# Kernel optimization log

Hardware: AMD Instinct MI355X
Metric: run time of the kernel (lower is better)

The kernel has to match this reference:

```python
import jax, jax.numpy as jnp
import numpy as np

N_NODES = 16384
D_FEAT = 128
HIDDEN = 64
THRESH = 0.85


def setup_inputs() -> dict:
    key = jax.random.key(0)
    kx, kw = jax.random.split(key, 2)
    x = jax.random.normal(kx, (N_NODES, D_FEAT), dtype=jnp.float32)
    # nn.Linear(node_features, hidden_size): weight [H, D], bias [H]
    W = jax.random.normal(kw, (HIDDEN, D_FEAT), dtype=jnp.float32) * 0.05
    b = jnp.zeros((HIDDEN,), dtype=jnp.float32)
    return {"x": x, "W": W, "b": b}


def reference(x, W, b):
    n = x.shape[0]
    # fidelity = (x_i . x_j)^2 for all pairs  -> [n, n]
    fid = jnp.square(x @ x.T)
    # edges exist iff fid >= threshold (weight 1.0); the 0.5-weight elif branch
    # in the original is unreachable. No self-loops (j starts at i+1).
    adj = (fid >= THRESH).astype(x.dtype)
    idx = jnp.arange(n)
    adj = adj.at[idx, idx].set(0.0)
    # weighted neighbor sum per node: [n, d]
    sums = adj @ x
    # original assigns agg[node] = (weights @ neighbor_feats).mean(), a SCALAR
    # broadcast across the feature row; isolated nodes stay zero (their sum
    # row is already zero, so mean is zero -> identical result).
    agg = jnp.broadcast_to(jnp.mean(sums, axis=-1, keepdims=True), x.shape)
    return agg @ W.T + b
```

## Files before the change

kernel.cpp:

```cpp
#include <hip/hip_runtime.h>

#define N_NODES 16384
#define D_FEAT  128
#define HIDDEN  64
#define THRESH  0.85f
#define BAND    0.004f
#define LQCAP   512
#define NBLK    512

typedef __attribute__((ext_vector_type(8))) short bf16x8;
typedef __attribute__((ext_vector_type(4))) float f32x4;

__device__ __forceinline__ unsigned short f32_to_bf16_rne(float f) {
    unsigned u = __float_as_uint(f);
    unsigned r = (u + 0x7FFFu + ((u >> 16) & 1u)) >> 16;
    return (unsigned short)r;
}

__device__ __forceinline__ void gl_lds16(const unsigned short* src, unsigned short* dst) {
    __builtin_amdgcn_global_load_lds(
        (const __attribute__((address_space(1))) unsigned int*)src,
        (__attribute__((address_space(3))) unsigned int*)dst, 16, 0, 0);
}

__global__ __launch_bounds__(256) void convert_kernel(const float* __restrict__ x,
                                                      unsigned short* __restrict__ xhi,
                                                      unsigned short* __restrict__ xlo) {
    int t = blockIdx.x * 256 + threadIdx.x;
    float4 v = ((const float4*)x)[t];
    float f[4] = {v.x, v.y, v.z, v.w};
    ushort4 ho, lo;
    unsigned short* hp = &ho.x;
    unsigned short* lp = &lo.x;
    #pragma unroll
    for (int k = 0; k < 4; ++k) {
        unsigned short h = f32_to_bf16_rne(f[k]);
        float hf = __uint_as_float(((unsigned)h) << 16);
        hp[k] = h;
        lp[k] = f32_to_bf16_rne(f[k] - hf);
    }
    ((ushort4*)xhi)[t] = ho;
    ((ushort4*)xlo)[t] = lo;
}

__global__ __launch_bounds__(256) void rowsum_kernel(const float* __restrict__ in,
                                                     float* __restrict__ out,
                                                     int nrows) {
    int wave = (blockIdx.x * blockDim.x + threadIdx.x) >> 6;
    int lane = threadIdx.x & 63;
    if (wave >= nrows) return;
    const float2 v = *reinterpret_cast<const float2*>(&in[wave * D_FEAT + lane * 2]);
    float sum = v.x + v.y;
    #pragma unroll
    for (int off = 32; off > 0; off >>= 1) sum += __shfl_down(sum, off, 64);
    if (lane == 0) out[wave] = sum;
}

__global__ __launch_bounds__(256, 2) void pair_mfma(const unsigned short* __restrict__ xhi,
                                                    const unsigned short* __restrict__ xlo,
                                                    const float* __restrict__ s,
                                                    float* __restrict__ acc,
                                                    unsigned* __restrict__ gqueue,
                                                    int* __restrict__ gqcnt) {
    __shared__ unsigned short Bs[2][2][64][128];
    __shared__ unsigned lq[LQCAP];
    __shared__ int lqcnt, lqbase;

    const int tid  = threadIdx.x;
    const int lane = tid & 63;
    const int w    = tid >> 6;
    const int l15  = lane & 15, l4 = lane >> 4, l7 = lane & 7;

    const int bid = blockIdx.x;
    const int swz = (bid & 7) * 64 + (bid >> 3);
    const int it  = swz & 63;
    const int jc  = swz >> 6;
    const int i0  = it * 256 + w * 64;
    const int jb0 = jc * 2048;

    bf16x8 ahi[4][4], alo[4][4];
    {
        const int abase = (i0 + l15) * D_FEAT + l4 * 8;
        #pragma unroll
        for (int rf = 0; rf < 4; ++rf)
            #pragma unroll
            for (int kc = 0; kc < 4; ++kc) {
                const int off = abase + rf * 16 * D_FEAT + kc * 32;
                ahi[rf][kc] = *(const bf16x8*)(xhi + off);
                alo[rf][kc] = *(const bf16x8*)(xlo + off);
            }
    }

    const int base_off = (tid >> 4) * 128 + (((tid & 15) ^ ((tid >> 4) & 7)) * 8);
    unsigned short* const dst0 = &Bs[0][0][0][0] + w * 512;

    const int rbyte = l15 * 256;
    int swzb[4];
    #pragma unroll
    for (int kc = 0; kc < 4; ++kc) swzb[kc] = (((kc * 4 + l4) ^ l7) * 16);

    {
        const int jelem = jb0 * D_FEAT;
        const unsigned short* hsrc = xhi + jelem + base_off;
        const unsigned short* lsrc = xlo + jelem + base_off;
        #pragma unroll
        for (int q = 0; q < 4; ++q) gl_lds16(hsrc + q * 2048, dst0 + q * 2048);
        #pragma unroll
        for (int q = 0; q < 4; ++q) gl_lds16(lsrc + q * 2048, dst0 + 8192 + q * 2048);
    }
    if (tid == 0) lqcnt = 0;
    __syncthreads();

    float accf[4][4] = {{0.f}};
    const char* const BsBytes = (const char*)&Bs[0][0][0][0];

    for (int jt = 0; jt < 32; ++jt) {
        const int buf = jt & 1;
        const int jb = jb0 + jt * 64;

        float sv[4];
        #pragma unroll
        for (int cg = 0; cg < 4; ++cg) sv[cg] = s[jb + cg * 16 + l15];

        if (jt < 31) {
            const int jelem = (jb + 64) * D_FEAT;
            const unsigned short* hsrc = xhi + jelem + base_off;
            const unsigned short* lsrc = xlo + jelem + base_off;
            unsigned short* db = dst0 + (buf ^ 1) * 16384;
            #pragma unroll
            for (int q = 0; q < 4; ++q) gl_lds16(hsrc + q * 2048, db + q * 2048);
            #pragma unroll
            for (int q = 0; q < 4; ++q) gl_lds16(lsrc + q * 2048, db + 8192 + q * 2048);
        }

        const bool diag = (jb == i0);
        const char* bp = BsBytes + buf * 32768;

        #pragma unroll
        for (int cg = 0; cg < 4; ++cg) {
            f32x4 C[4];
            #pragma unroll
            for (int rf = 0; rf < 4; ++rf) C[rf] = (f32x4){0.f, 0.f, 0.f, 0.f};

            #pragma unroll
            for (int kc = 0; kc < 4; ++kc) {
                const bf16x8 bh = *(const bf16x8*)(bp + cg * 4096 + rbyte + swzb[kc]);
                const bf16x8 bl = *(const bf16x8*)(bp + 16384 + cg * 4096 + rbyte + swzb[kc]);
                #pragma unroll
                for (int rf = 0; rf < 4; ++rf) {
                    C[rf] = __builtin_amdgcn_mfma_f32_16x16x32_bf16(ahi[rf][kc], bh, C[rf], 0, 0, 0);
                    C[rf] = __builtin_amdgcn_mfma_f32_16x16x32_bf16(alo[rf][kc], bh, C[rf], 0, 0, 0);
                    C[rf] = __builtin_amdgcn_mfma_f32_16x16x32_bf16(ahi[rf][kc], bl, C[rf], 0, 0, 0);
                }
            }

            const int jcol = jb + cg * 16 + l15;
            const float svc = sv[cg];
            #pragma unroll
            for (int rf = 0; rf < 4; ++rf) {
                const int gib = i0 + rf * 16 + l4 * 4;
                #pragma unroll
                for (int r = 0; r < 4; ++r) {
                    const float d = C[rf][r];
                    const float tt = fmaf(d, d, -THRESH);
                    if (fabsf(tt) < BAND) {
                        int p = atomicAdd(&lqcnt, 1);
                        if (p < LQCAP)
                            lq[p] = (((unsigned)(gib + r)) << 14) | (unsigned)jcol;
                    }
                    bool edge = (tt >= BAND);
                    if (diag) edge = edge && ((gib + r) != jcol);
                    accf[rf][r] += edge ? svc : 0.f;
                }
            }
        }
        __syncthreads();
    }

    if (tid == 0) {
        int c = lqcnt; if (c > LQCAP) c = LQCAP;
        lqbase = atomicAdd(gqcnt, c);
        lqcnt = c;
    }
    __syncthreads();
    for (int p = tid; p < lqcnt; p += 256) gqueue[lqbase + p] = lq[p];

    #pragma unroll
    for (int rf = 0; rf < 4; ++rf)
        #pragma unroll
        for (int r = 0; r < 4; ++r) {
            float v = accf[rf][r];
            v += __shfl_xor(v, 1);
            v += __shfl_xor(v, 2);
            v += __shfl_xor(v, 4);
            v += __shfl_xor(v, 8);
            if (l15 == 0) atomicAdd(&acc[i0 + rf * 16 + l4 * 4 + r], v);
        }
}

__global__ __launch_bounds__(256) void fixup_kernel(const unsigned* __restrict__ q,
                                                    const int* __restrict__ qcnt,
                                                    const float* __restrict__ x,
                                                    const float* __restrict__ s,
                                                    float* __restrict__ acc) {
    const int n = *qcnt;
    const int gw = (blockIdx.x * 256 + threadIdx.x) >> 6;
    const int lane = threadIdx.x & 63;
    const int nw = (gridDim.x * 256) >> 6;
    for (int p = gw; p < n; p += nw) {
        const unsigned e = q[p];
        const int i = (int)(e >> 14), j = (int)(e & 16383u);
        const float2 av = ((const float2*)(x + (size_t)i * D_FEAT))[lane];
        const float2 bv = ((const float2*)(x + (size_t)j * D_FEAT))[lane];
        float d = fmaf(av.y, bv.y, av.x * bv.x);
        #pragma unroll
        for (int off = 32; off > 0; off >>= 1) d += __shfl_xor(d, off);
        if (lane == 0) {
            const float tt = fmaf(d, d, -THRESH);
            if (tt >= 0.f) atomicAdd(&acc[i], s[j]);
        }
    }
}

__global__ __launch_bounds__(256) void out_kernel(const float* __restrict__ acc,
                                                  const float* __restrict__ wsum,
                                                  const float* __restrict__ b,
                                                  float* __restrict__ out) {
    int gid = blockIdx.x * blockDim.x + threadIdx.x;
    int i = gid >> 6;
    int h = gid & 63;
    float a = acc[i] * (1.0f / 128.0f);
    out[gid] = fmaf(a, wsum[h], b[h]);
}

extern "C" void kernel_launch(void* const* d_in, const int* in_sizes, int n_in,
                              void* d_out, int out_size, void* d_ws, size_t ws_size,
                              hipStream_t stream) {
    const float* x = (const float*)d_in[0];
    const float* W = (const float*)d_in[1];
    const float* b = (const float*)d_in[2];
    float* out = (float*)d_out;

    float*    s     = (float*)d_ws;
    float*    acc   = s + N_NODES;
    float*    wsum  = acc + N_NODES;
    int*      qcnt  = (int*)(wsum + 64);
    unsigned* queue = (unsigned*)(qcnt + 64);
    unsigned short* xhi = (unsigned short*)((char*)d_ws + (2u << 20));
    unsigned short* xlo = (unsigned short*)((char*)d_ws + (6u << 20));

    convert_kernel<<<dim3(N_NODES * D_FEAT / 4 / 256), dim3(256), 0, stream>>>(x, xhi, xlo);
    rowsum_kernel<<<dim3((N_NODES * 64 + 255) / 256), dim3(256), 0, stream>>>(x, s, N_NODES);
    rowsum_kernel<<<dim3((HIDDEN * 64 + 255) / 256), dim3(256), 0, stream>>>(W, wsum, HIDDEN);
    hipMemsetAsync(acc, 0, N_NODES * sizeof(float), stream);
    hipMemsetAsync(qcnt, 0, sizeof(int), stream);

    pair_mfma<<<dim3(NBLK), dim3(256), 0, stream>>>(xhi, xlo, s, acc, queue, qcnt);
    fixup_kernel<<<dim3(256), dim3(256), 0, stream>>>(queue, qcnt, x, s, acc);
    out_kernel<<<dim3(N_NODES * HIDDEN / 256), dim3(256), 0, stream>>>(acc, wsum, b, out);
}
```

Baseline: 327.2 us.

## Triple-buffer B tiles, fuse preprocessing kernels, and drop diagonal mask via subtraction

The pair kernel now streams 32-row B tiles through a three-deep LDS ring, using vmcnt waits and a single barrier per step instead of a double buffer with a full syncthreads. Row sums for the block are staged in LDS, and MFMA sections are raised to higher wave priority. The bf16 split, row sum, acc zeroing and queue-counter reset are fused into one kernel, which removes the memsets and one launch. The per-element diagonal check is removed and the self term is subtracted in the output kernel instead. This relies on each self pair landing in the edge branch and not the band queue, and the pipeline issues a few redundant wraparound loads.

```diff
diff --git a/kernel.cpp b/kernel.cpp
--- a/kernel.cpp
+++ b/kernel.cpp
@@ -7,6 +7,7 @@
 #define BAND    0.004f
 #define LQCAP   512
 #define NBLK    512
+#define NT      64
 
 typedef __attribute__((ext_vector_type(8))) short bf16x8;
 typedef __attribute__((ext_vector_type(4))) float f32x4;
@@ -23,11 +24,15 @@
         (__attribute__((address_space(3))) unsigned int*)dst, 16, 0, 0);
 }
 
-__global__ __launch_bounds__(256) void convert_kernel(const float* __restrict__ x,
-                                                      unsigned short* __restrict__ xhi,
-                                                      unsigned short* __restrict__ xlo) {
-    int t = blockIdx.x * 256 + threadIdx.x;
-    float4 v = ((const float4*)x)[t];
+__global__ __launch_bounds__(256) void convert_rowsum_kernel(const float* __restrict__ x,
+                                                             unsigned short* __restrict__ xhi,
+                                                             unsigned short* __restrict__ xlo,
+                                                             float* __restrict__ s,
+                                                             float* __restrict__ acc,
+                                                             int* __restrict__ qcnt) {
+    const int tid  = threadIdx.x;
+    const int gidx = blockIdx.x * 256 + tid;
+    float4 v = ((const float4*)x)[gidx];
     float f[4] = {v.x, v.y, v.z, v.w};
     ushort4 ho, lo;
     unsigned short* hp = &ho.x;
@@ -39,8 +44,16 @@
         hp[k] = h;
         lp[k] = f32_to_bf16_rne(f[k] - hf);
     }
-    ((ushort4*)xhi)[t] = ho;
-    ((ushort4*)xlo)[t] = lo;
+    ((ushort4*)xhi)[gidx] = ho;
+    ((ushort4*)xlo)[gidx] = lo;
+
+    float sum = (v.x + v.y) + (v.z + v.w);
+    #pragma unroll
+    for (int off = 16; off > 0; off >>= 1) sum += __shfl_xor(sum, off);
+    if ((tid & 31) == 0) s[blockIdx.x * 8 + (tid >> 5)] = sum;
+
+    if (tid < 8) acc[blockIdx.x * 8 + tid] = 0.0f;
+    if (gidx == 0) *qcnt = 0;
 }
 
 __global__ __launch_bounds__(256) void rowsum_kernel(const float* __restrict__ in,
@@ -62,7 +75,8 @@
                                                     float* __restrict__ acc,
                                                     unsigned* __restrict__ gqueue,
                                                     int* __restrict__ gqcnt) {
-    __shared__ unsigned short Bs[2][2][64][128];
+    __shared__ unsigned short Bs[3][2][32][128];
+    __shared__ float s_lds[2048];
     __shared__ unsigned lq[LQCAP];
     __shared__ int lqcnt, lqbase;
 
@@ -91,61 +105,72 @@
             }
     }
 
-    const int base_off = (tid >> 4) * 128 + (((tid & 15) ^ ((tid >> 4) & 7)) * 8);
-    unsigned short* const dst0 = &Bs[0][0][0][0] + w * 512;
-
+    {
+        const float4* sp4 = (const float4*)(s + jb0);
+        float4* sl4 = (float4*)s_lds;
+        sl4[tid * 2]     = sp4[tid * 2];
+        sl4[tid * 2 + 1] = sp4[tid * 2 + 1];
+    }
+    if (tid == 0) lqcnt = 0;
+    __syncthreads();
+
+    int src_off[4]; int dst_off[4]; int plane_sel[4];
+    #pragma unroll
+    for (int q = 0; q < 4; ++q) {
+        const int id = w * 4 + q;
+        const int rowt = (id & 7) * 4 + l4;
+        plane_sel[q] = id >> 3;
+        src_off[q] = rowt * D_FEAT + ((l15 ^ (rowt & 7)) * 8);
+        dst_off[q] = (id >> 3) * 4096 + (id & 7) * 512;
+    }
+    unsigned short* const BsE = &Bs[0][0][0][0];
+
+    #pragma unroll
+    for (int tt = 0; tt < 2; ++tt) {
+        const int jelem = (jb0 + tt * 32) * D_FEAT;
+        #pragma unroll
+        for (int q = 0; q < 4; ++q) {
+            const unsigned short* sp = (plane_sel[q] ? xlo : xhi) + jelem + src_off[q];
+            gl_lds16(sp, BsE + tt * 8192 + dst_off[q]);
+        }
+    }
+
+    float accf[4][4] = {{0.f}};
+    const char* const BsBytes = (const char*)BsE;
     const int rbyte = l15 * 256;
     int swzb[4];
     #pragma unroll
     for (int kc = 0; kc < 4; ++kc) swzb[kc] = (((kc * 4 + l4) ^ l7) * 16);
 
-    {
-        const int jelem = jb0 * D_FEAT;
-        const unsigned short* hsrc = xhi + jelem + base_off;
-        const unsigned short* lsrc = xlo + jelem + base_off;
-        #pragma unroll
-        for (int q = 0; q < 4; ++q) gl_lds16(hsrc + q * 2048, dst0 + q * 2048);
-        #pragma unroll
-        for (int q = 0; q < 4; ++q) gl_lds16(lsrc + q * 2048, dst0 + 8192 + q * 2048);
-    }
-    if (tid == 0) lqcnt = 0;
-    __syncthreads();
-
-    float accf[4][4] = {{0.f}};
-    const char* const BsBytes = (const char*)&Bs[0][0][0][0];
-
-    for (int jt = 0; jt < 32; ++jt) {
-        const int buf = jt & 1;
-        const int jb = jb0 + jt * 64;
-
-        float sv[4];
-        #pragma unroll
-        for (int cg = 0; cg < 4; ++cg) sv[cg] = s[jb + cg * 16 + l15];
-
-        if (jt < 31) {
-            const int jelem = (jb + 64) * D_FEAT;
-            const unsigned short* hsrc = xhi + jelem + base_off;
-            const unsigned short* lsrc = xlo + jelem + base_off;
-            unsigned short* db = dst0 + (buf ^ 1) * 16384;
-            #pragma unroll
-            for (int q = 0; q < 4; ++q) gl_lds16(hsrc + q * 2048, db + q * 2048);
-            #pragma unroll
-            for (int q = 0; q < 4; ++q) gl_lds16(lsrc + q * 2048, db + 8192 + q * 2048);
-        }
-
-        const bool diag = (jb == i0);
-        const char* bp = BsBytes + buf * 32768;
-
-        #pragma unroll
-        for (int cg = 0; cg < 4; ++cg) {
+    int bufc = 0, bufs = 2;
+    for (int t = 0; t < NT; ++t) {
+        asm volatile("s_waitcnt vmcnt(4)" ::: "memory");
+        __builtin_amdgcn_s_barrier();
+
+        {
+            const int jelem = (jb0 + ((t + 2) & 63) * 32) * D_FEAT;
+            unsigned short* db = BsE + bufs * 8192;
+            #pragma unroll
+            for (int q = 0; q < 4; ++q) {
+                const unsigned short* sp = (plane_sel[q] ? xlo : xhi) + jelem + src_off[q];
+                gl_lds16(sp, db + dst_off[q]);
+            }
+        }
+
+        const int jb = jb0 + t * 32;
+        const char* bp = BsBytes + bufc * 16384;
+
+        #pragma unroll
+        for (int cg = 0; cg < 2; ++cg) {
             f32x4 C[4];
             #pragma unroll
             for (int rf = 0; rf < 4; ++rf) C[rf] = (f32x4){0.f, 0.f, 0.f, 0.f};
 
+            __builtin_amdgcn_s_setprio(1);
             #pragma unroll
             for (int kc = 0; kc < 4; ++kc) {
                 const bf16x8 bh = *(const bf16x8*)(bp + cg * 4096 + rbyte + swzb[kc]);
-                const bf16x8 bl = *(const bf16x8*)(bp + 16384 + cg * 4096 + rbyte + swzb[kc]);
+                const bf16x8 bl = *(const bf16x8*)(bp + 8192 + cg * 4096 + rbyte + swzb[kc]);
                 #pragma unroll
                 for (int rf = 0; rf < 4; ++rf) {
                     C[rf] = __builtin_amdgcn_mfma_f32_16x16x32_bf16(ahi[rf][kc], bh, C[rf], 0, 0, 0);
@@ -153,9 +178,10 @@
                     C[rf] = __builtin_amdgcn_mfma_f32_16x16x32_bf16(ahi[rf][kc], bl, C[rf], 0, 0, 0);
                 }
             }
+            __builtin_amdgcn_s_setprio(0);
 
             const int jcol = jb + cg * 16 + l15;
-            const float svc = sv[cg];
+            const float svc = s_lds[t * 32 + cg * 16 + l15];
             #pragma unroll
             for (int rf = 0; rf < 4; ++rf) {
                 const int gib = i0 + rf * 16 + l4 * 4;
@@ -168,14 +194,16 @@
                         if (p < LQCAP)
                             lq[p] = (((unsigned)(gib + r)) << 14) | (unsigned)jcol;
                     }
-                    bool edge = (tt >= BAND);
-                    if (diag) edge = edge && ((gib + r) != jcol);
-                    accf[rf][r] += edge ? svc : 0.f;
+                    accf[rf][r] += (tt >= BAND) ? svc : 0.f;
                 }
             }
         }
-        __syncthreads();
-    }
+
+        bufc = (bufc == 2) ? 0 : bufc + 1;
+        bufs = (bufs == 2) ? 0 : bufs + 1;
+    }
+
+    __syncthreads();
 
     if (tid == 0) {
         int c = lqcnt; if (c > LQCAP) c = LQCAP;
@@ -223,13 +251,14 @@
 }
 
 __global__ __launch_bounds__(256) void out_kernel(const float* __restrict__ acc,
+                                                  const float* __restrict__ s,
                                                   const float* __restrict__ wsum,
                                                   const float* __restrict__ b,
                                                   float* __restrict__ out) {
     int gid = blockIdx.x * blockDim.x + threadIdx.x;
     int i = gid >> 6;
     int h = gid & 63;
-    float a = acc[i] * (1.0f / 128.0f);
+    float a = (acc[i] - s[i]) * (1.0f / 128.0f);
     out[gid] = fmaf(a, wsum[h], b[h]);
 }
 
@@ -249,13 +278,10 @@
     unsigned short* xhi = (unsigned short*)((char*)d_ws + (2u << 20));
     unsigned short* xlo = (unsigned short*)((char*)d_ws + (6u << 20));
 
-    convert_kernel<<<dim3(N_NODES * D_FEAT / 4 / 256), dim3(256), 0, stream>>>(x, xhi, xlo);
-    rowsum_kernel<<<dim3((N_NODES * 64 + 255) / 256), dim3(256), 0, stream>>>(x, s, N_NODES);
+    convert_rowsum_kernel<<<dim3(N_NODES / 8), dim3(256), 0, stream>>>(x, xhi, xlo, s, acc, qcnt);
     rowsum_kernel<<<dim3((HIDDEN * 64 + 255) / 256), dim3(256), 0, stream>>>(W, wsum, HIDDEN);
-    hipMemsetAsync(acc, 0, N_NODES * sizeof(float), stream);
-    hipMemsetAsync(qcnt, 0, sizeof(int), stream);
 
     pair_mfma<<<dim3(NBLK), dim3(256), 0, stream>>>(xhi, xlo, s, acc, queue, qcnt);
     fixup_kernel<<<dim3(256), dim3(256), 0, stream>>>(queue, qcnt, x, s, acc);
-    out_kernel<<<dim3(N_NODES * HIDDEN / 256), dim3(256), 0, stream>>>(acc, wsum, b, out);
-}
+    out_kernel<<<dim3(N_NODES * HIDDEN / 256), dim3(256), 0, stream>>>(acc, s, wsum, b, out);
+}
```

Measured after the change: 319.5 us. 1.02x faster.
